# Kernel optimization log

Hardware: AMD Instinct MI355X
Metric: run time of the kernel (lower is better)

Reference implementation:

```python
import jax, jax.numpy as jnp
import numpy as np

N, C, B = 32, 1024, 1024
EPS = 1e-12


def setup_inputs() -> dict:
    key = jax.random.key(0)
    k1, k2, k3 = jax.random.split(key, 3)
    X = jax.random.normal(k1, (N, C, B), dtype=jnp.float32)
    # xavier_uniform for square [C, C]: bound = sqrt(6/(C+C))
    bound = float(np.sqrt(6.0 / (C + C)))
    Wk = jax.random.uniform(k2, (C, C), minval=-bound, maxval=bound, dtype=jnp.float32)
    Wq = jax.random.uniform(k3, (C, C), minval=-bound, maxval=bound, dtype=jnp.float32)
    Wk0 = jnp.zeros((C, 1), dtype=jnp.float32)
    Wq0 = jnp.zeros((C, 1), dtype=jnp.float32)
    return {"X": X, "Wk": Wk, "Wq": Wq, "Wk0": Wk0, "Wq0": Wq0}


def reference(X, Wk, Wq, Wk0, Wq0):
    # X: [N, C, B]; Wk/Wq: [C, C]; Wk0/Wq0: [C, 1]
    K = jnp.einsum('cd,ndb->ncb', Wk, X) + Wk0  # [N, C, B]
    Q = jnp.einsum('cd,ndb->ncb', Wq, X) + Wq0  # [N, C, B]
    DK2 = jnp.sum(K * K, axis=1)                # [N, B]
    DQ2 = jnp.sum(Q * Q, axis=1)                # [N, B]
    DQK = jnp.sqrt(jnp.maximum(DQ2[:, :, None] * DK2[:, None, :], EPS))  # [N, B, B]
    Y = jnp.einsum('ncq,nck->nqk', Q, K) / DQK  # [N, B, B]
    SM = jax.nn.softmax(Y, axis=1)              # column-wise softmax (dim=1)
    Z = jnp.einsum('ncb,nbq->ncq', X, SM)       # [N, C, B]
    return Z
```

## Files before the change

kernel.cpp:

```cpp
#include <hip/hip_runtime.h>


typedef __bf16 bf16x8 __attribute__((ext_vector_type(8)));
typedef float  f32x4  __attribute__((ext_vector_type(4)));

#define LOAD16_LDS(g, l)                                                       \
  __builtin_amdgcn_global_load_lds(                                            \
      (const __attribute__((address_space(1))) void*)(g),                      \
      (__attribute__((address_space(3))) void*)(l), 16, 0, 0)

#define FENCE() asm volatile("" ::: "memory")
#define SBAR()                                                                 \
  do { FENCE(); __builtin_amdgcn_s_barrier(); FENCE(); } while (0)
#define LGKM0()                                                                \
  do { asm volatile("s_waitcnt lgkmcnt(0)" ::: "memory");                      \
       __builtin_amdgcn_sched_barrier(0); } while (0)
#define VMW(n)                                                                 \
  do { asm volatile("s_waitcnt vmcnt(" #n ")" ::: "memory");                   \
       __builtin_amdgcn_sched_barrier(0); } while (0)
#define MFMA16(a, b, c) __builtin_amdgcn_mfma_f32_16x16x32_bf16((a), (b), (c), 0, 0, 0)

__global__ __launch_bounds__(256) void convert_w(
    const float* __restrict__ Wk, const float* __restrict__ Wq,
    const float* __restrict__ Wk0, const float* __restrict__ Wq0,
    __bf16* __restrict__ Wb, float* __restrict__ bias2) {
  int i = blockIdx.x * 256 + threadIdx.x;
  if (i < 1048576) Wb[i] = (__bf16)Wk[i];
  else             Wb[i] = (__bf16)Wq[i - 1048576];
  if (i < 1024) bias2[i] = Wk0[i];
  if (i >= 1048576 && i < 1048576 + 1024) bias2[1024 + (i - 1048576)] = Wq0[i - 1048576];
}

__global__ __launch_bounds__(256) void convert_x(
    const float* __restrict__ X, __bf16* __restrict__ Xb, __bf16* __restrict__ Xtb) {
  const int n = blockIdx.z;
  const int c0 = blockIdx.y * 32, b0 = blockIdx.x * 32;
  __shared__ float t[32][33];
  const int tx = threadIdx.x, ty = threadIdx.y;
  const float* Xn = X + (size_t)n * 1024 * 1024;
  __bf16* Xbn = Xb + (size_t)n * 1024 * 1024;
  __bf16* Xtn = Xtb + (size_t)n * 1024 * 1024;
#pragma unroll
  for (int i = 0; i < 4; ++i) {
    int c = c0 + ty + i * 8;
    float v = Xn[(size_t)c * 1024 + b0 + tx];
    Xbn[(size_t)c * 1024 + b0 + tx] = (__bf16)v;
    t[ty + i * 8][tx] = v;
  }
  __syncthreads();
#pragma unroll
  for (int i = 0; i < 4; ++i) {
    int b = b0 + ty + i * 8;
    Xtn[(size_t)b * 1024 + c0 + tx] = (__bf16)t[tx][ty + i * 8];
  }
}

template <int EPI>
__global__ __launch_bounds__(512) void gemm256(
    const __bf16* __restrict__ A, const __bf16* __restrict__ Bm,
    void* __restrict__ Out, int lda, int ldb, int ldo, int K,
    long long sA, long long sB, long long sO,
    const float* __restrict__ rowS, const float* __restrict__ colS,
    const float* __restrict__ bias,
    float* __restrict__ sq0, float* __restrict__ sq1) {
  extern __shared__ char smem[];
  const int n = blockIdx.z;
  A += (size_t)n * sA;
  Bm += (size_t)n * sB;
  const int tileM = blockIdx.y * 256, tileN = blockIdx.x * 256;

  const int tid = threadIdx.x;
  const int w = tid >> 6, lane = tid & 63;
  const int wm = w >> 2, wn = w & 3;
  const int r16 = lane & 15, q16 = lane >> 4;
  const int wb = w * 1024;

  const int srow = tid >> 3;
  const int scol8 = ((tid & 7) ^ (srow & 7)) * 8;
  const __bf16* gA[4];
  const __bf16* gB[4];
#pragma unroll
  for (int c = 0; c < 4; ++c) {
    gA[c] = A + (size_t)(tileM + c * 64 + srow) * lda + scol8;
    gB[c] = Bm + (size_t)(tileN + c * 64 + srow) * ldb + scol8;
  }

  const int sw = (r16 & 7) << 4;
  const int cc0 = (q16 * 16) ^ sw;
  const int cc1 = cc0 ^ 64;
  const int aRow = (wm * 128 + r16) * 128;
  const int bRow = (wn * 64 + r16) * 128;

  f32x4 acc[8][4];
#pragma unroll
  for (int i = 0; i < 8; ++i)
#pragma unroll
    for (int j = 0; j < 4; ++j) acc[i][j] = (f32x4){0.f, 0.f, 0.f, 0.f};

  const int NT = K >> 6;

  {
    char* A0 = smem;
    char* B0 = smem + 32768;
    char* A1 = smem + 65536;
    char* B1 = smem + 65536 + 32768;
    LOAD16_LDS(gB[0], B0 + 0 * 8192 + wb);
    LOAD16_LDS(gB[1], B0 + 1 * 8192 + wb);
    FENCE();
    LOAD16_LDS(gB[2], B0 + 2 * 8192 + wb);
    LOAD16_LDS(gB[3], B0 + 3 * 8192 + wb);
    FENCE();
    LOAD16_LDS(gA[0], A0 + 0 * 8192 + wb);
    LOAD16_LDS(gA[2], A0 + 2 * 8192 + wb);
    FENCE();
    LOAD16_LDS(gA[1], A0 + 1 * 8192 + wb);
    LOAD16_LDS(gA[3], A0 + 3 * 8192 + wb);
    FENCE();
    LOAD16_LDS(gB[0] + 64, B1 + 0 * 8192 + wb);
    LOAD16_LDS(gB[1] + 64, B1 + 1 * 8192 + wb);
    FENCE();
    LOAD16_LDS(gB[2] + 64, B1 + 2 * 8192 + wb);
    LOAD16_LDS(gB[3] + 64, B1 + 3 * 8192 + wb);
    FENCE();
    LOAD16_LDS(gA[0] + 64, A1 + 0 * 8192 + wb);
    LOAD16_LDS(gA[2] + 64, A1 + 2 * 8192 + wb);
    VMW(6);
    SBAR();
  }

  int kU3 = 64, kU0 = 128, kU1 = 128, kU2 = 128;

  for (int t = 0; t < NT; ++t) {
    char* Ab = smem + (size_t)((t & 1) * 65536);
    char* Bb = Ab + 32768;
    char* An = smem + (size_t)(((t & 1) ^ 1) * 65536);

    bf16x8 bfr[4][2];
#pragma unroll
    for (int ni = 0; ni < 4; ++ni) {
      bfr[ni][0] = *(const bf16x8*)(Bb + bRow + ni * 2048 + cc0);
      bfr[ni][1] = *(const bf16x8*)(Bb + bRow + ni * 2048 + cc1);
    }

#pragma unroll
    for (int p = 0; p < 4; ++p) {
      bf16x8 af[2][2];
#pragma unroll
      for (int j = 0; j < 2; ++j) {
        af[j][0] = *(const bf16x8*)(Ab + aRow + (2 * p + j) * 2048 + cc0);
        af[j][1] = *(const bf16x8*)(Ab + aRow + (2 * p + j) * 2048 + cc1);
      }
      if (p == 0) {
        if (kU3 < K) {
          LOAD16_LDS(gA[1] + kU3, An + 1 * 8192 + wb);
          LOAD16_LDS(gA[3] + kU3, An + 3 * 8192 + wb);
          kU3 += 64;
        }
      } else if (p == 1) {
        if (kU0 < K) {
          LOAD16_LDS(gB[0] + kU0, Bb + 0 * 8192 + wb);
          LOAD16_LDS(gB[1] + kU0, Bb + 1 * 8192 + wb);
          kU0 += 64;
        }
      } else if (p == 2) {
        if (kU1 < K) {
          LOAD16_LDS(gB[2] + kU1, Bb + 2 * 8192 + wb);
          LOAD16_LDS(gB[3] + kU1, Bb + 3 * 8192 + wb);
          kU1 += 64;
        }
      } else {
        if (kU2 < K) {
          LOAD16_LDS(gA[0] + kU2, Ab + 0 * 8192 + wb);
          LOAD16_LDS(gA[2] + kU2, Ab + 2 * 8192 + wb);
          kU2 += 64;
        }
        if (t < NT - 2) { VMW(6); } else { VMW(0); }
      }
      SBAR();
      LGKM0();
      __builtin_amdgcn_s_setprio(1);
#pragma unroll
      for (int ni = 0; ni < 4; ++ni) {
#pragma unroll
        for (int j = 0; j < 2; ++j) {
          acc[2 * p + j][ni] = MFMA16(af[j][0], bfr[ni][0], acc[2 * p + j][ni]);
          acc[2 * p + j][ni] = MFMA16(af[j][1], bfr[ni][1], acc[2 * p + j][ni]);
        }
      }
      __builtin_amdgcn_s_setprio(0);
      SBAR();
    }
  }

  const int rowBase = tileM + wm * 128;
  const int colBase = tileN + wn * 64;
  if (EPI == 0) {
    float* sqp = (tileN < 1024) ? sq0 : sq1;
    float bs[4];
#pragma unroll
    for (int ni = 0; ni < 4; ++ni) bs[ni] = bias[colBase + ni * 16 + r16];
#pragma unroll
    for (int mi = 0; mi < 8; ++mi) {
#pragma unroll
      for (int t_ = 0; t_ < 4; ++t_) {
        const int grow = rowBase + mi * 16 + q16 * 4 + t_;
        float ss = 0.f;
#pragma unroll
        for (int ni = 0; ni < 4; ++ni) {
          const int gcol = colBase + ni * 16 + r16;
          const __bf16 bv = (__bf16)(acc[mi][ni][t_] + bs[ni]);
          ((__bf16*)Out)[(size_t)n * sO + (size_t)grow * ldo + gcol] = bv;
          const float f = (float)bv;
          ss += f * f;
        }
        ss += __shfl_xor(ss, 1);
        ss += __shfl_xor(ss, 2);
        ss += __shfl_xor(ss, 4);
        ss += __shfl_xor(ss, 8);
        if (r16 == 0) atomicAdd(&sqp[n * 1024 + grow], ss);
      }
    }
  } else if (EPI == 1) {
    float cs[4];
#pragma unroll
    for (int ni = 0; ni < 4; ++ni)
      cs[ni] = colS[n * 1024 + colBase + ni * 16 + r16];
#pragma unroll
    for (int mi = 0; mi < 8; ++mi) {
#pragma unroll
      for (int t_ = 0; t_ < 4; ++t_) {
        const int grow = rowBase + mi * 16 + q16 * 4 + t_;
        const float rs = rowS[n * 1024 + grow];
        float ss = 0.f;
#pragma unroll
        for (int ni = 0; ni < 4; ++ni) {
          const int gcol = colBase + ni * 16 + r16;
          const float y = acc[mi][ni][t_] * rsqrtf(fmaxf(rs * cs[ni], 1e-12f));
          const __bf16 e = (__bf16)__expf(y - 1.0f);
          ((__bf16*)Out)[(size_t)n * sO + (size_t)grow * ldo + gcol] = e;
          ss += (float)e;
        }
        ss += __shfl_xor(ss, 1);
        ss += __shfl_xor(ss, 2);
        ss += __shfl_xor(ss, 4);
        ss += __shfl_xor(ss, 8);
        if (r16 == 0) atomicAdd(&sq0[n * 1024 + grow], ss);
      }
    }
  } else {
    float inv[4];
#pragma unroll
    for (int ni = 0; ni < 4; ++ni)
      inv[ni] = 1.0f / colS[n * 1024 + colBase + ni * 16 + r16];
#pragma unroll
    for (int mi = 0; mi < 8; ++mi)
#pragma unroll
      for (int ni = 0; ni < 4; ++ni)
#pragma unroll
        for (int t_ = 0; t_ < 4; ++t_) {
          const int grow = rowBase + mi * 16 + q16 * 4 + t_;
          const int gcol = colBase + ni * 16 + r16;
          ((float*)Out)[(size_t)n * sO + (size_t)grow * ldo + gcol] =
              acc[mi][ni][t_] * inv[ni];
        }
  }
}

extern "C" void kernel_launch(void* const* d_in, const int* in_sizes, int n_in,
                              void* d_out, int out_size, void* d_ws, size_t ws_size,
                              hipStream_t stream) {
  const float* X   = (const float*)d_in[0];
  const float* Wk  = (const float*)d_in[1];
  const float* Wq  = (const float*)d_in[2];
  const float* Wk0 = (const float*)d_in[3];
  const float* Wq0 = (const float*)d_in[4];

  char* ws = (char*)d_ws;
  const size_t MB = 1ull << 20;
  __bf16* Xb   = (__bf16*)(ws);
  __bf16* Xtb  = (__bf16*)(ws + 64 * MB);
  __bf16* ET   = (__bf16*)(ws + 64 * MB);
  __bf16* Wb   = (__bf16*)(ws + 128 * MB);
  __bf16* KQT  = (__bf16*)(ws + 132 * MB);
  float*  DK2  = (float*)(ws + 260 * MB);
  float*  DQ2  = (float*)(ws + 260 * MB + 128 * 1024);
  float*  S    = (float*)(ws + 260 * MB + 256 * 1024);
  float*  bias2= (float*)(ws + 260 * MB + 384 * 1024);

  const long long M1 = 1024LL * 1024LL;

  hipFuncSetAttribute(reinterpret_cast<const void*>(&gemm256<0>),
                      hipFuncAttributeMaxDynamicSharedMemorySize, 131072);
  hipFuncSetAttribute(reinterpret_cast<const void*>(&gemm256<1>),
                      hipFuncAttributeMaxDynamicSharedMemorySize, 131072);
  hipFuncSetAttribute(reinterpret_cast<const void*>(&gemm256<2>),
                      hipFuncAttributeMaxDynamicSharedMemorySize, 131072);

  hipMemsetAsync(DK2, 0, 3 * 128 * 1024, stream);

  convert_w<<<8192, 256, 0, stream>>>(Wk, Wq, Wk0, Wq0, Wb, bias2);
  convert_x<<<dim3(32, 32, 32), dim3(32, 8), 0, stream>>>(X, Xb, Xtb);

  gemm256<0><<<dim3(8, 4, 32), 512, 131072, stream>>>(
      Xtb, Wb, KQT, 1024, 1024, 2048, 1024, M1, 0LL, 2 * M1,
      nullptr, nullptr, bias2, DK2, DQ2);

  gemm256<1><<<dim3(4, 4, 32), 512, 131072, stream>>>(
      KQT, KQT + 1024, ET, 2048, 2048, 1024, 1024, 2 * M1, 2 * M1, M1,
      DK2, DQ2, nullptr, S, nullptr);

  gemm256<2><<<dim3(4, 4, 32), 512, 131072, stream>>>(
      Xb, ET, (float*)d_out, 1024, 1024, 1024, 1024, M1, M1, M1,
      nullptr, S, nullptr, nullptr, nullptr);
}
```

Baseline: 580.9 us.

## Make GEMM blocks persistent over several N-tiles with cross-tile prefetch

Each GEMM block now processes IPB consecutive output tiles along N, launched as a flat grid of 256 blocks (one per CU). During the last K iteration of one tile, it prefetches the first K-slices of the next tile's B and A operands into the free LDS buffer, so the next tile's pipeline starts warm and the epilogue overlaps with loading. This cuts the number of waves and the pipeline ramp-up per tile, and keeps the A row tile resident across iterations. The trade-off is a serial chain of tiles per block, with a full vmcnt wait after each epilogue and more fragile waitcnt accounting.

```diff
diff --git a/kernel.cpp b/kernel.cpp
--- a/kernel.cpp
+++ b/kernel.cpp
@@ -55,7 +55,7 @@
   }
 }
 
-template <int EPI>
+template <int EPI, int IPB, int GXS>
 __global__ __launch_bounds__(512) void gemm256(
     const __bf16* __restrict__ A, const __bf16* __restrict__ Bm,
     void* __restrict__ Out, int lda, int ldb, int ldo, int K,
@@ -64,10 +64,14 @@
     const float* __restrict__ bias,
     float* __restrict__ sq0, float* __restrict__ sq1) {
   extern __shared__ char smem[];
-  const int n = blockIdx.z;
+
+  const int baseid = blockIdx.x * IPB;
+  const int tN0   = (baseid & ((1 << GXS) - 1)) * 256;
+  const int tileM = ((baseid >> GXS) & 3) * 256;
+  const int n     = baseid >> (GXS + 2);
+
   A += (size_t)n * sA;
   Bm += (size_t)n * sB;
-  const int tileM = blockIdx.y * 256, tileN = blockIdx.x * 256;
 
   const int tid = threadIdx.x;
   const int w = tid >> 6, lane = tid & 63;
@@ -82,8 +86,9 @@
 #pragma unroll
   for (int c = 0; c < 4; ++c) {
     gA[c] = A + (size_t)(tileM + c * 64 + srow) * lda + scol8;
-    gB[c] = Bm + (size_t)(tileN + c * 64 + srow) * ldb + scol8;
+    gB[c] = Bm + (size_t)(tN0 + c * 64 + srow) * ldb + scol8;
   }
+  const long long bStep = 256LL * ldb;
 
   const int sw = (r16 & 7) << 4;
   const int cc0 = (q16 * 16) ^ sw;
@@ -91,178 +96,215 @@
   const int aRow = (wm * 128 + r16) * 128;
   const int bRow = (wn * 64 + r16) * 128;
 
-  f32x4 acc[8][4];
-#pragma unroll
-  for (int i = 0; i < 8; ++i)
-#pragma unroll
-    for (int j = 0; j < 4; ++j) acc[i][j] = (f32x4){0.f, 0.f, 0.f, 0.f};
-
   const int NT = K >> 6;
 
-  {
+#pragma unroll 1
+  for (int it = 0; it < IPB; ++it) {
+    const int tileN = tN0 + it * 256;
+    const bool pre = (it + 1 < IPB);
+
+    f32x4 acc[8][4];
+#pragma unroll
+    for (int i = 0; i < 8; ++i)
+#pragma unroll
+      for (int j = 0; j < 4; ++j) acc[i][j] = (f32x4){0.f, 0.f, 0.f, 0.f};
+
     char* A0 = smem;
     char* B0 = smem + 32768;
     char* A1 = smem + 65536;
     char* B1 = smem + 65536 + 32768;
-    LOAD16_LDS(gB[0], B0 + 0 * 8192 + wb);
-    LOAD16_LDS(gB[1], B0 + 1 * 8192 + wb);
-    FENCE();
-    LOAD16_LDS(gB[2], B0 + 2 * 8192 + wb);
-    LOAD16_LDS(gB[3], B0 + 3 * 8192 + wb);
-    FENCE();
-    LOAD16_LDS(gA[0], A0 + 0 * 8192 + wb);
-    LOAD16_LDS(gA[2], A0 + 2 * 8192 + wb);
-    FENCE();
-    LOAD16_LDS(gA[1], A0 + 1 * 8192 + wb);
-    LOAD16_LDS(gA[3], A0 + 3 * 8192 + wb);
-    FENCE();
-    LOAD16_LDS(gB[0] + 64, B1 + 0 * 8192 + wb);
-    LOAD16_LDS(gB[1] + 64, B1 + 1 * 8192 + wb);
-    FENCE();
-    LOAD16_LDS(gB[2] + 64, B1 + 2 * 8192 + wb);
-    LOAD16_LDS(gB[3] + 64, B1 + 3 * 8192 + wb);
-    FENCE();
-    LOAD16_LDS(gA[0] + 64, A1 + 0 * 8192 + wb);
-    LOAD16_LDS(gA[2] + 64, A1 + 2 * 8192 + wb);
-    VMW(6);
-    SBAR();
-  }
-
-  int kU3 = 64, kU0 = 128, kU1 = 128, kU2 = 128;
-
-  for (int t = 0; t < NT; ++t) {
-    char* Ab = smem + (size_t)((t & 1) * 65536);
-    char* Bb = Ab + 32768;
-    char* An = smem + (size_t)(((t & 1) ^ 1) * 65536);
-
-    bf16x8 bfr[4][2];
-#pragma unroll
-    for (int ni = 0; ni < 4; ++ni) {
-      bfr[ni][0] = *(const bf16x8*)(Bb + bRow + ni * 2048 + cc0);
-      bfr[ni][1] = *(const bf16x8*)(Bb + bRow + ni * 2048 + cc1);
-    }
-
-#pragma unroll
-    for (int p = 0; p < 4; ++p) {
-      bf16x8 af[2][2];
-#pragma unroll
-      for (int j = 0; j < 2; ++j) {
-        af[j][0] = *(const bf16x8*)(Ab + aRow + (2 * p + j) * 2048 + cc0);
-        af[j][1] = *(const bf16x8*)(Ab + aRow + (2 * p + j) * 2048 + cc1);
-      }
-      if (p == 0) {
-        if (kU3 < K) {
-          LOAD16_LDS(gA[1] + kU3, An + 1 * 8192 + wb);
-          LOAD16_LDS(gA[3] + kU3, An + 3 * 8192 + wb);
-          kU3 += 64;
-        }
-      } else if (p == 1) {
-        if (kU0 < K) {
-          LOAD16_LDS(gB[0] + kU0, Bb + 0 * 8192 + wb);
-          LOAD16_LDS(gB[1] + kU0, Bb + 1 * 8192 + wb);
-          kU0 += 64;
-        }
-      } else if (p == 2) {
-        if (kU1 < K) {
-          LOAD16_LDS(gB[2] + kU1, Bb + 2 * 8192 + wb);
-          LOAD16_LDS(gB[3] + kU1, Bb + 3 * 8192 + wb);
-          kU1 += 64;
-        }
-      } else {
-        if (kU2 < K) {
-          LOAD16_LDS(gA[0] + kU2, Ab + 0 * 8192 + wb);
-          LOAD16_LDS(gA[2] + kU2, Ab + 2 * 8192 + wb);
-          kU2 += 64;
-        }
-        if (t < NT - 2) { VMW(6); } else { VMW(0); }
-      }
+
+    if (it == 0) {
+      LOAD16_LDS(gB[0], B0 + 0 * 8192 + wb);
+      LOAD16_LDS(gB[1], B0 + 1 * 8192 + wb);
+      FENCE();
+      LOAD16_LDS(gB[2], B0 + 2 * 8192 + wb);
+      LOAD16_LDS(gB[3], B0 + 3 * 8192 + wb);
+      FENCE();
+      LOAD16_LDS(gA[0], A0 + 0 * 8192 + wb);
+      LOAD16_LDS(gA[2], A0 + 2 * 8192 + wb);
+      FENCE();
+      LOAD16_LDS(gA[1], A0 + 1 * 8192 + wb);
+      LOAD16_LDS(gA[3], A0 + 3 * 8192 + wb);
+      FENCE();
+      LOAD16_LDS(gB[0] + 64, B1 + 0 * 8192 + wb);
+      LOAD16_LDS(gB[1] + 64, B1 + 1 * 8192 + wb);
+      FENCE();
+      LOAD16_LDS(gB[2] + 64, B1 + 2 * 8192 + wb);
+      LOAD16_LDS(gB[3] + 64, B1 + 3 * 8192 + wb);
+      FENCE();
+      LOAD16_LDS(gA[0] + 64, A1 + 0 * 8192 + wb);
+      LOAD16_LDS(gA[2] + 64, A1 + 2 * 8192 + wb);
+      VMW(6);
       SBAR();
-      LGKM0();
-      __builtin_amdgcn_s_setprio(1);
-#pragma unroll
-      for (int ni = 0; ni < 4; ++ni) {
-#pragma unroll
-        for (int j = 0; j < 2; ++j) {
-          acc[2 * p + j][ni] = MFMA16(af[j][0], bfr[ni][0], acc[2 * p + j][ni]);
-          acc[2 * p + j][ni] = MFMA16(af[j][1], bfr[ni][1], acc[2 * p + j][ni]);
-        }
-      }
-      __builtin_amdgcn_s_setprio(0);
+    } else {
+      LOAD16_LDS(gB[0] + 64, B1 + 0 * 8192 + wb);
+      LOAD16_LDS(gB[1] + 64, B1 + 1 * 8192 + wb);
+      FENCE();
+      LOAD16_LDS(gB[2] + 64, B1 + 2 * 8192 + wb);
+      LOAD16_LDS(gB[3] + 64, B1 + 3 * 8192 + wb);
+      FENCE();
+      LOAD16_LDS(gA[0] + 64, A1 + 0 * 8192 + wb);
+      LOAD16_LDS(gA[2] + 64, A1 + 2 * 8192 + wb);
       SBAR();
     }
-  }
-
-  const int rowBase = tileM + wm * 128;
-  const int colBase = tileN + wn * 64;
-  if (EPI == 0) {
-    float* sqp = (tileN < 1024) ? sq0 : sq1;
-    float bs[4];
-#pragma unroll
-    for (int ni = 0; ni < 4; ++ni) bs[ni] = bias[colBase + ni * 16 + r16];
-#pragma unroll
-    for (int mi = 0; mi < 8; ++mi) {
-#pragma unroll
-      for (int t_ = 0; t_ < 4; ++t_) {
-        const int grow = rowBase + mi * 16 + q16 * 4 + t_;
-        float ss = 0.f;
+
+    int kU3 = 64, kU0 = 128, kU1 = 128, kU2 = 128;
+
+    for (int t = 0; t < NT; ++t) {
+      char* Ab = smem + (size_t)((t & 1) * 65536);
+      char* Bb = Ab + 32768;
+      char* An = smem + (size_t)(((t & 1) ^ 1) * 65536);
+      char* Bn = An + 32768;
+
+      bf16x8 bfr[4][2];
+#pragma unroll
+      for (int ni = 0; ni < 4; ++ni) {
+        bfr[ni][0] = *(const bf16x8*)(Bb + bRow + ni * 2048 + cc0);
+        bfr[ni][1] = *(const bf16x8*)(Bb + bRow + ni * 2048 + cc1);
+      }
+
+#pragma unroll
+      for (int p = 0; p < 4; ++p) {
+        bf16x8 af[2][2];
+#pragma unroll
+        for (int j = 0; j < 2; ++j) {
+          af[j][0] = *(const bf16x8*)(Ab + aRow + (2 * p + j) * 2048 + cc0);
+          af[j][1] = *(const bf16x8*)(Ab + aRow + (2 * p + j) * 2048 + cc1);
+        }
+        if (p == 0) {
+          if (kU3 < K) {
+            LOAD16_LDS(gA[1] + kU3, An + 1 * 8192 + wb);
+            LOAD16_LDS(gA[3] + kU3, An + 3 * 8192 + wb);
+            kU3 += 64;
+          } else if (pre && t == NT - 1) {
+            LOAD16_LDS(gB[0] + bStep, Bn + 0 * 8192 + wb);
+            LOAD16_LDS(gB[1] + bStep, Bn + 1 * 8192 + wb);
+          }
+        } else if (p == 1) {
+          if (kU0 < K) {
+            LOAD16_LDS(gB[0] + kU0, Bb + 0 * 8192 + wb);
+            LOAD16_LDS(gB[1] + kU0, Bb + 1 * 8192 + wb);
+            kU0 += 64;
+          } else if (pre && t == NT - 1) {
+            LOAD16_LDS(gB[2] + bStep, Bn + 2 * 8192 + wb);
+            LOAD16_LDS(gB[3] + bStep, Bn + 3 * 8192 + wb);
+          }
+        } else if (p == 2) {
+          if (kU1 < K) {
+            LOAD16_LDS(gB[2] + kU1, Bb + 2 * 8192 + wb);
+            LOAD16_LDS(gB[3] + kU1, Bb + 3 * 8192 + wb);
+            kU1 += 64;
+          } else if (pre && t == NT - 1) {
+            LOAD16_LDS(gA[0], An + 0 * 8192 + wb);
+            LOAD16_LDS(gA[2], An + 2 * 8192 + wb);
+          }
+        } else {
+          if (kU2 < K) {
+            LOAD16_LDS(gA[0] + kU2, Ab + 0 * 8192 + wb);
+            LOAD16_LDS(gA[2] + kU2, Ab + 2 * 8192 + wb);
+            kU2 += 64;
+          } else if (pre && t == NT - 1) {
+            LOAD16_LDS(gA[1], An + 1 * 8192 + wb);
+            LOAD16_LDS(gA[3], An + 3 * 8192 + wb);
+          }
+          if (t <= NT - 3)      { VMW(6); }
+          else if (t == NT - 2) { VMW(0); }
+        }
+        SBAR();
+        LGKM0();
+        __builtin_amdgcn_s_setprio(1);
 #pragma unroll
         for (int ni = 0; ni < 4; ++ni) {
-          const int gcol = colBase + ni * 16 + r16;
-          const __bf16 bv = (__bf16)(acc[mi][ni][t_] + bs[ni]);
-          ((__bf16*)Out)[(size_t)n * sO + (size_t)grow * ldo + gcol] = bv;
-          const float f = (float)bv;
-          ss += f * f;
-        }
-        ss += __shfl_xor(ss, 1);
-        ss += __shfl_xor(ss, 2);
-        ss += __shfl_xor(ss, 4);
-        ss += __shfl_xor(ss, 8);
-        if (r16 == 0) atomicAdd(&sqp[n * 1024 + grow], ss);
+#pragma unroll
+          for (int j = 0; j < 2; ++j) {
+            acc[2 * p + j][ni] = MFMA16(af[j][0], bfr[ni][0], acc[2 * p + j][ni]);
+            acc[2 * p + j][ni] = MFMA16(af[j][1], bfr[ni][1], acc[2 * p + j][ni]);
+          }
+        }
+        __builtin_amdgcn_s_setprio(0);
+        SBAR();
       }
     }
-  } else if (EPI == 1) {
-    float cs[4];
-#pragma unroll
-    for (int ni = 0; ni < 4; ++ni)
-      cs[ni] = colS[n * 1024 + colBase + ni * 16 + r16];
-#pragma unroll
-    for (int mi = 0; mi < 8; ++mi) {
-#pragma unroll
-      for (int t_ = 0; t_ < 4; ++t_) {
-        const int grow = rowBase + mi * 16 + q16 * 4 + t_;
-        const float rs = rowS[n * 1024 + grow];
-        float ss = 0.f;
-#pragma unroll
-        for (int ni = 0; ni < 4; ++ni) {
-          const int gcol = colBase + ni * 16 + r16;
-          const float y = acc[mi][ni][t_] * rsqrtf(fmaxf(rs * cs[ni], 1e-12f));
-          const __bf16 e = (__bf16)__expf(y - 1.0f);
-          ((__bf16*)Out)[(size_t)n * sO + (size_t)grow * ldo + gcol] = e;
-          ss += (float)e;
-        }
-        ss += __shfl_xor(ss, 1);
-        ss += __shfl_xor(ss, 2);
-        ss += __shfl_xor(ss, 4);
-        ss += __shfl_xor(ss, 8);
-        if (r16 == 0) atomicAdd(&sq0[n * 1024 + grow], ss);
-      }
-    }
-  } else {
-    float inv[4];
-#pragma unroll
-    for (int ni = 0; ni < 4; ++ni)
-      inv[ni] = 1.0f / colS[n * 1024 + colBase + ni * 16 + r16];
-#pragma unroll
-    for (int mi = 0; mi < 8; ++mi)
-#pragma unroll
-      for (int ni = 0; ni < 4; ++ni)
+
+    const int rowBase = tileM + wm * 128;
+    const int colBase = tileN + wn * 64;
+    if (EPI == 0) {
+      float* sqp = (tileN < 1024) ? sq0 : sq1;
+      float bs[4];
+#pragma unroll
+      for (int ni = 0; ni < 4; ++ni) bs[ni] = bias[colBase + ni * 16 + r16];
+#pragma unroll
+      for (int mi = 0; mi < 8; ++mi) {
 #pragma unroll
         for (int t_ = 0; t_ < 4; ++t_) {
           const int grow = rowBase + mi * 16 + q16 * 4 + t_;
-          const int gcol = colBase + ni * 16 + r16;
-          ((float*)Out)[(size_t)n * sO + (size_t)grow * ldo + gcol] =
-              acc[mi][ni][t_] * inv[ni];
-        }
+          float ss = 0.f;
+#pragma unroll
+          for (int ni = 0; ni < 4; ++ni) {
+            const int gcol = colBase + ni * 16 + r16;
+            const __bf16 bv = (__bf16)(acc[mi][ni][t_] + bs[ni]);
+            ((__bf16*)Out)[(size_t)n * sO + (size_t)grow * ldo + gcol] = bv;
+            const float f = (float)bv;
+            ss += f * f;
+          }
+          ss += __shfl_xor(ss, 1);
+          ss += __shfl_xor(ss, 2);
+          ss += __shfl_xor(ss, 4);
+          ss += __shfl_xor(ss, 8);
+          if (r16 == 0) atomicAdd(&sqp[n * 1024 + grow], ss);
+        }
+      }
+    } else if (EPI == 1) {
+      float cs[4];
+#pragma unroll
+      for (int ni = 0; ni < 4; ++ni)
+        cs[ni] = colS[n * 1024 + colBase + ni * 16 + r16];
+#pragma unroll
+      for (int mi = 0; mi < 8; ++mi) {
+#pragma unroll
+        for (int t_ = 0; t_ < 4; ++t_) {
+          const int grow = rowBase + mi * 16 + q16 * 4 + t_;
+          const float rs = rowS[n * 1024 + grow];
+          float ss = 0.f;
+#pragma unroll
+          for (int ni = 0; ni < 4; ++ni) {
+            const int gcol = colBase + ni * 16 + r16;
+            const float y = acc[mi][ni][t_] * rsqrtf(fmaxf(rs * cs[ni], 1e-12f));
+            const __bf16 e = (__bf16)__expf(y - 1.0f);
+            ((__bf16*)Out)[(size_t)n * sO + (size_t)grow * ldo + gcol] = e;
+            ss += (float)e;
+          }
+          ss += __shfl_xor(ss, 1);
+          ss += __shfl_xor(ss, 2);
+          ss += __shfl_xor(ss, 4);
+          ss += __shfl_xor(ss, 8);
+          if (r16 == 0) atomicAdd(&sq0[n * 1024 + grow], ss);
+        }
+      }
+    } else {
+      float inv[4];
+#pragma unroll
+      for (int ni = 0; ni < 4; ++ni)
+        inv[ni] = 1.0f / colS[n * 1024 + colBase + ni * 16 + r16];
+#pragma unroll
+      for (int mi = 0; mi < 8; ++mi)
+#pragma unroll
+        for (int ni = 0; ni < 4; ++ni)
+#pragma unroll
+          for (int t_ = 0; t_ < 4; ++t_) {
+            const int grow = rowBase + mi * 16 + q16 * 4 + t_;
+            const int gcol = colBase + ni * 16 + r16;
+            ((float*)Out)[(size_t)n * sO + (size_t)grow * ldo + gcol] =
+                acc[mi][ni][t_] * inv[ni];
+          }
+    }
+
+    if (pre) {
+      VMW(0);
+#pragma unroll
+      for (int c = 0; c < 4; ++c) gB[c] += bStep;
+    }
   }
 }
 
@@ -289,11 +331,11 @@
 
   const long long M1 = 1024LL * 1024LL;
 
-  hipFuncSetAttribute(reinterpret_cast<const void*>(&gemm256<0>),
+  hipFuncSetAttribute(reinterpret_cast<const void*>(&gemm256<0, 4, 3>),
                       hipFuncAttributeMaxDynamicSharedMemorySize, 131072);
-  hipFuncSetAttribute(reinterpret_cast<const void*>(&gemm256<1>),
+  hipFuncSetAttribute(reinterpret_cast<const void*>(&gemm256<1, 2, 2>),
                       hipFuncAttributeMaxDynamicSharedMemorySize, 131072);
-  hipFuncSetAttribute(reinterpret_cast<const void*>(&gemm256<2>),
+  hipFuncSetAttribute(reinterpret_cast<const void*>(&gemm256<2, 2, 2>),
                       hipFuncAttributeMaxDynamicSharedMemorySize, 131072);
 
   hipMemsetAsync(DK2, 0, 3 * 128 * 1024, stream);
@@ -301,15 +343,15 @@
   convert_w<<<8192, 256, 0, stream>>>(Wk, Wq, Wk0, Wq0, Wb, bias2);
   convert_x<<<dim3(32, 32, 32), dim3(32, 8), 0, stream>>>(X, Xb, Xtb);
 
-  gemm256<0><<<dim3(8, 4, 32), 512, 131072, stream>>>(
+  gemm256<0, 4, 3><<<dim3(256), 512, 131072, stream>>>(
       Xtb, Wb, KQT, 1024, 1024, 2048, 1024, M1, 0LL, 2 * M1,
       nullptr, nullptr, bias2, DK2, DQ2);
 
-  gemm256<1><<<dim3(4, 4, 32), 512, 131072, stream>>>(
+  gemm256<1, 2, 2><<<dim3(256), 512, 131072, stream>>>(
       KQT, KQT + 1024, ET, 2048, 2048, 1024, 1024, 2 * M1, 2 * M1, M1,
       DK2, DQ2, nullptr, S, nullptr);
 
-  gemm256<2><<<dim3(4, 4, 32), 512, 131072, stream>>>(
+  gemm256<2, 2, 2><<<dim3(256), 512, 131072, stream>>>(
       Xb, ET, (float*)d_out, 1024, 1024, 1024, 1024, M1, M1, M1,
       nullptr, S, nullptr, nullptr, nullptr);
 }
```

After: 659.0 us. +13.4%, slower.

## Pad bf16 workspace row strides and defer X conversion to reuse KQT buffer

Applied to the files above, without the earlier changes.

Row strides of the bf16 intermediates change from 1024/2048 to 1032/2056 elements, likely to break power-of-two strides that cause cache-set or channel conflicts in the GEMM tile loads. The plain bf16 copy of X is split out of the transpose kernel into a separate vectorised kernel. That kernel runs after the second GEMM so its output can overwrite the now-dead KQT buffer and shrink the workspace. The cost is an extra launch and a second read of X.

```diff
diff --git a/kernel.cpp b/kernel.cpp
--- a/kernel.cpp
+++ b/kernel.cpp
@@ -20,6 +20,11 @@
        __builtin_amdgcn_sched_barrier(0); } while (0)
 #define MFMA16(a, b, c) __builtin_amdgcn_mfma_f32_16x16x32_bf16((a), (b), (c), 0, 0, 0)
 
+#define LDX 1032
+#define LDK 2056
+#define SX  (1024LL * LDX)
+#define SK  (1024LL * LDK)
+
 __global__ __launch_bounds__(256) void convert_w(
     const float* __restrict__ Wk, const float* __restrict__ Wq,
     const float* __restrict__ Wk0, const float* __restrict__ Wq0,
@@ -32,27 +37,34 @@
 }
 
 __global__ __launch_bounds__(256) void convert_x(
-    const float* __restrict__ X, __bf16* __restrict__ Xb, __bf16* __restrict__ Xtb) {
+    const float* __restrict__ X, __bf16* __restrict__ Xtb) {
   const int n = blockIdx.z;
   const int c0 = blockIdx.y * 32, b0 = blockIdx.x * 32;
   __shared__ float t[32][33];
   const int tx = threadIdx.x, ty = threadIdx.y;
   const float* Xn = X + (size_t)n * 1024 * 1024;
-  __bf16* Xbn = Xb + (size_t)n * 1024 * 1024;
-  __bf16* Xtn = Xtb + (size_t)n * 1024 * 1024;
+  __bf16* Xtn = Xtb + (size_t)n * SX;
 #pragma unroll
   for (int i = 0; i < 4; ++i) {
     int c = c0 + ty + i * 8;
-    float v = Xn[(size_t)c * 1024 + b0 + tx];
-    Xbn[(size_t)c * 1024 + b0 + tx] = (__bf16)v;
-    t[ty + i * 8][tx] = v;
+    t[ty + i * 8][tx] = Xn[(size_t)c * 1024 + b0 + tx];
   }
   __syncthreads();
 #pragma unroll
   for (int i = 0; i < 4; ++i) {
     int b = b0 + ty + i * 8;
-    Xtn[(size_t)b * 1024 + c0 + tx] = (__bf16)t[tx][ty + i * 8];
-  }
+    Xtn[(size_t)b * LDX + c0 + tx] = (__bf16)t[tx][ty + i * 8];
+  }
+}
+
+__global__ __launch_bounds__(256) void convert_xb(
+    const float* __restrict__ X, __bf16* __restrict__ Xb) {
+  const int c = blockIdx.x, n = blockIdx.y;
+  const float* src = X + ((size_t)n * 1024 + c) * 1024 + threadIdx.x * 4;
+  __bf16* dst = Xb + (size_t)n * SX + (size_t)c * LDX + threadIdx.x * 4;
+  float4 v = *(const float4*)src;
+  __bf16 o[4] = {(__bf16)v.x, (__bf16)v.y, (__bf16)v.z, (__bf16)v.w};
+  *(ushort4*)dst = *(const ushort4*)o;
 }
 
 template <int EPI>
@@ -276,18 +288,15 @@
   const float* Wq0 = (const float*)d_in[4];
 
   char* ws = (char*)d_ws;
-  const size_t MB = 1ull << 20;
-  __bf16* Xb   = (__bf16*)(ws);
-  __bf16* Xtb  = (__bf16*)(ws + 64 * MB);
-  __bf16* ET   = (__bf16*)(ws + 64 * MB);
-  __bf16* Wb   = (__bf16*)(ws + 128 * MB);
-  __bf16* KQT  = (__bf16*)(ws + 132 * MB);
-  float*  DK2  = (float*)(ws + 260 * MB);
-  float*  DQ2  = (float*)(ws + 260 * MB + 128 * 1024);
-  float*  S    = (float*)(ws + 260 * MB + 256 * 1024);
-  float*  bias2= (float*)(ws + 260 * MB + 384 * 1024);
-
-  const long long M1 = 1024LL * 1024LL;
+  float*  DK2  = (float*)(ws);
+  float*  DQ2  = (float*)(ws + 131072);
+  float*  S    = (float*)(ws + 262144);
+  float*  bias2= (float*)(ws + 393216);
+  __bf16* Xtb  = (__bf16*)(ws + 524288);
+  __bf16* ET   = (__bf16*)(ws + 524288);
+  __bf16* Wb   = (__bf16*)(ws + 68157440ull);
+  __bf16* KQT  = (__bf16*)(ws + 72351744ull);
+  __bf16* Xb   = (__bf16*)(ws + 72351744ull);
 
   hipFuncSetAttribute(reinterpret_cast<const void*>(&gemm256<0>),
                       hipFuncAttributeMaxDynamicSharedMemorySize, 131072);
@@ -296,20 +305,22 @@
   hipFuncSetAttribute(reinterpret_cast<const void*>(&gemm256<2>),
                       hipFuncAttributeMaxDynamicSharedMemorySize, 131072);
 
-  hipMemsetAsync(DK2, 0, 3 * 128 * 1024, stream);
+  hipMemsetAsync(DK2, 0, 3 * 131072, stream);
 
   convert_w<<<8192, 256, 0, stream>>>(Wk, Wq, Wk0, Wq0, Wb, bias2);
-  convert_x<<<dim3(32, 32, 32), dim3(32, 8), 0, stream>>>(X, Xb, Xtb);
+  convert_x<<<dim3(32, 32, 32), dim3(32, 8), 0, stream>>>(X, Xtb);
 
   gemm256<0><<<dim3(8, 4, 32), 512, 131072, stream>>>(
-      Xtb, Wb, KQT, 1024, 1024, 2048, 1024, M1, 0LL, 2 * M1,
+      Xtb, Wb, KQT, LDX, 1024, LDK, 1024, SX, 0LL, SK,
       nullptr, nullptr, bias2, DK2, DQ2);
 
   gemm256<1><<<dim3(4, 4, 32), 512, 131072, stream>>>(
-      KQT, KQT + 1024, ET, 2048, 2048, 1024, 1024, 2 * M1, 2 * M1, M1,
+      KQT, KQT + 1024, ET, LDK, LDK, LDX, 1024, SK, SK, SX,
       DK2, DQ2, nullptr, S, nullptr);
 
+  convert_xb<<<dim3(1024, 32), 256, 0, stream>>>(X, Xb);
+
   gemm256<2><<<dim3(4, 4, 32), 512, 131072, stream>>>(
-      Xb, ET, (float*)d_out, 1024, 1024, 1024, 1024, M1, M1, M1,
+      Xb, ET, (float*)d_out, LDX, LDX, 1024, 1024, SX, SX, 1024LL * 1024LL,
       nullptr, S, nullptr, nullptr, nullptr);
 }
```

After: 643.9 us. 1.11x slower.

## Run the K/Q projection and QK^T GEMMs in FP8 instead of BF16

Applied to the files above, without the earlier changes.

Converts W and transposed X to FP8 e4m3 and adds a new FP8 MFMA GEMM kernel, with a 64-byte K tile and a different LDS swizzle, for the projection and score GEMMs. The K/Q intermediate is also stored in FP8. The final X·softmax GEMM stays BF16. This halves the operand bytes and uses the higher-throughput FP8 MFMA, at the cost of much lower precision in the normalized dot products, which feed an exp and may hurt accuracy.

```diff
diff --git a/kernel.cpp b/kernel.cpp
--- a/kernel.cpp
+++ b/kernel.cpp
@@ -19,27 +19,32 @@
   do { asm volatile("s_waitcnt vmcnt(" #n ")" ::: "memory");                   \
        __builtin_amdgcn_sched_barrier(0); } while (0)
 #define MFMA16(a, b, c) __builtin_amdgcn_mfma_f32_16x16x32_bf16((a), (b), (c), 0, 0, 0)
+#define MFMA8(a, b, c)  __builtin_amdgcn_mfma_f32_16x16x32_fp8_fp8((a), (b), (c), 0, 0, 0)
+
+#define F32_TO_FP8PK(a, b) __builtin_amdgcn_cvt_pk_fp8_f32((a), (b), 0, false)
+#define FP8_TO_F32(p, s)   __builtin_amdgcn_cvt_f32_fp8((p), (s))
 
 __global__ __launch_bounds__(256) void convert_w(
     const float* __restrict__ Wk, const float* __restrict__ Wq,
     const float* __restrict__ Wk0, const float* __restrict__ Wq0,
-    __bf16* __restrict__ Wb, float* __restrict__ bias2) {
+    unsigned char* __restrict__ W8, float* __restrict__ bias2) {
   int i = blockIdx.x * 256 + threadIdx.x;
-  if (i < 1048576) Wb[i] = (__bf16)Wk[i];
-  else             Wb[i] = (__bf16)Wq[i - 1048576];
+  float v = (i < 1048576) ? Wk[i] : Wq[i - 1048576];
+  W8[i] = (unsigned char)(F32_TO_FP8PK(v, v) & 0xff);
   if (i < 1024) bias2[i] = Wk0[i];
   if (i >= 1048576 && i < 1048576 + 1024) bias2[1024 + (i - 1048576)] = Wq0[i - 1048576];
 }
 
 __global__ __launch_bounds__(256) void convert_x(
-    const float* __restrict__ X, __bf16* __restrict__ Xb, __bf16* __restrict__ Xtb) {
+    const float* __restrict__ X, __bf16* __restrict__ Xb,
+    unsigned char* __restrict__ Xt8) {
   const int n = blockIdx.z;
   const int c0 = blockIdx.y * 32, b0 = blockIdx.x * 32;
   __shared__ float t[32][33];
   const int tx = threadIdx.x, ty = threadIdx.y;
   const float* Xn = X + (size_t)n * 1024 * 1024;
   __bf16* Xbn = Xb + (size_t)n * 1024 * 1024;
-  __bf16* Xtn = Xtb + (size_t)n * 1024 * 1024;
+  unsigned char* Xtn = Xt8 + (size_t)n * 1024 * 1024;
 #pragma unroll
   for (int i = 0; i < 4; ++i) {
     int c = c0 + ty + i * 8;
@@ -51,13 +56,14 @@
 #pragma unroll
   for (int i = 0; i < 4; ++i) {
     int b = b0 + ty + i * 8;
-    Xtn[(size_t)b * 1024 + c0 + tx] = (__bf16)t[tx][ty + i * 8];
+    float v = t[tx][ty + i * 8];
+    Xtn[(size_t)b * 1024 + c0 + tx] = (unsigned char)(F32_TO_FP8PK(v, v) & 0xff);
   }
 }
 
 template <int EPI>
-__global__ __launch_bounds__(512) void gemm256(
-    const __bf16* __restrict__ A, const __bf16* __restrict__ Bm,
+__global__ __launch_bounds__(512) void gemm_fp8(
+    const unsigned char* __restrict__ A, const unsigned char* __restrict__ Bm,
     void* __restrict__ Out, int lda, int ldb, int ldo, int K,
     long long sA, long long sB, long long sO,
     const float* __restrict__ rowS, const float* __restrict__ colS,
@@ -69,8 +75,171 @@
   Bm += (size_t)n * sB;
   const int tileM = blockIdx.y * 256, tileN = blockIdx.x * 256;
 
-  const int tid = threadIdx.x;
-  const int w = tid >> 6, lane = tid & 63;
+  const int tid = threadIdx.x, w = tid >> 6, lane = tid & 63;
+  const int wm = w >> 2, wn = w & 3;
+  const int r16 = lane & 15, q16 = lane >> 4;
+
+  const int hf = w >> 2, wq = w & 3;
+  const int srow = wq * 16 + (lane >> 2);
+  const int scol = (((lane & 3) ^ ((lane >> 2) & 3) ^ ((lane >> 4) & 3)) << 4);
+  const unsigned char* gA2 = A + (size_t)(tileM + hf * 128 + srow) * lda + scol;
+  const unsigned char* gA3 = A + (size_t)(tileM + 64 + hf * 128 + srow) * lda + scol;
+  const unsigned char* gB0 = Bm + (size_t)(tileN + hf * 64 + srow) * ldb + scol;
+  const unsigned char* gB1 = Bm + (size_t)(tileN + 128 + hf * 64 + srow) * ldb + scol;
+  const int dA2 = hf * 8192 + wq * 1024;
+  const int dA3 = dA2 + 4096;
+  const int dB0 = hf * 4096 + wq * 1024;
+  const int dB1 = dB0 + 8192;
+
+  const int s16 = (r16 & 3) ^ ((r16 >> 2) & 3);
+  const int cc0 = (((q16 >> 1) ^ s16) << 4) + ((q16 & 1) << 3);
+  const int cc1 = cc0 ^ 32;
+  const int aRow = (wm * 128 + r16) * 64;
+  const int bRow = (wn * 64 + r16) * 64;
+
+  f32x4 acc[8][4];
+#pragma unroll
+  for (int i = 0; i < 8; ++i)
+#pragma unroll
+    for (int j = 0; j < 4; ++j) acc[i][j] = (f32x4){0.f, 0.f, 0.f, 0.f};
+
+  const int NT = K >> 6;
+
+  {
+    char* A0 = smem;
+    char* B0 = smem + 16384;
+    char* A1 = smem + 32768;
+    char* B1 = A1 + 16384;
+    LOAD16_LDS(gB0, B0 + dB0); FENCE();
+    LOAD16_LDS(gB1, B0 + dB1); FENCE();
+    LOAD16_LDS(gA2, A0 + dA2); FENCE();
+    LOAD16_LDS(gA3, A0 + dA3); FENCE();
+    LOAD16_LDS(gB0 + 64, B1 + dB0); FENCE();
+    LOAD16_LDS(gB1 + 64, B1 + dB1); FENCE();
+    LOAD16_LDS(gA2 + 64, A1 + dA2);
+    VMW(3);
+    SBAR();
+  }
+
+  int kU3 = 64, kU0 = 128, kU1 = 128, kU2 = 128;
+
+  for (int t = 0; t < NT; ++t) {
+    char* Ab = smem + (size_t)((t & 1) * 32768);
+    char* Bb = Ab + 16384;
+    char* An = smem + (size_t)(((t & 1) ^ 1) * 32768);
+
+    long bfr[4][2];
+#pragma unroll
+    for (int ni = 0; ni < 4; ++ni) {
+      bfr[ni][0] = *(const long*)(Bb + bRow + ni * 1024 + cc0);
+      bfr[ni][1] = *(const long*)(Bb + bRow + ni * 1024 + cc1);
+    }
+
+#pragma unroll
+    for (int p = 0; p < 4; ++p) {
+      long af[2][2];
+#pragma unroll
+      for (int j = 0; j < 2; ++j) {
+        af[j][0] = *(const long*)(Ab + aRow + (2 * p + j) * 1024 + cc0);
+        af[j][1] = *(const long*)(Ab + aRow + (2 * p + j) * 1024 + cc1);
+      }
+      if (p == 0) {
+        if (kU3 < K) { LOAD16_LDS(gA3 + kU3, An + dA3); kU3 += 64; }
+      } else if (p == 1) {
+        if (kU0 < K) { LOAD16_LDS(gB0 + kU0, Bb + dB0); kU0 += 64; }
+      } else if (p == 2) {
+        if (kU1 < K) { LOAD16_LDS(gB1 + kU1, Bb + dB1); kU1 += 64; }
+      } else {
+        if (kU2 < K) { LOAD16_LDS(gA2 + kU2, Ab + dA2); kU2 += 64; }
+        if (t < NT - 2) { VMW(3); } else { VMW(0); }
+      }
+      SBAR();
+      LGKM0();
+      __builtin_amdgcn_s_setprio(1);
+#pragma unroll
+      for (int ni = 0; ni < 4; ++ni) {
+#pragma unroll
+        for (int j = 0; j < 2; ++j) {
+          acc[2 * p + j][ni] = MFMA8(af[j][0], bfr[ni][0], acc[2 * p + j][ni]);
+          acc[2 * p + j][ni] = MFMA8(af[j][1], bfr[ni][1], acc[2 * p + j][ni]);
+        }
+      }
+      __builtin_amdgcn_s_setprio(0);
+      SBAR();
+    }
+  }
+
+  const int rowBase = tileM + wm * 128;
+  const int colBase = tileN + wn * 64;
+  if (EPI == 0) {
+    float* sqp = (tileN < 1024) ? sq0 : sq1;
+    float bs[4];
+#pragma unroll
+    for (int ni = 0; ni < 4; ++ni) bs[ni] = bias[colBase + ni * 16 + r16];
+#pragma unroll
+    for (int mi = 0; mi < 8; ++mi) {
+#pragma unroll
+      for (int t_ = 0; t_ < 4; ++t_) {
+        const int grow = rowBase + mi * 16 + q16 * 4 + t_;
+        const int p01 = F32_TO_FP8PK(acc[mi][0][t_] + bs[0], acc[mi][1][t_] + bs[1]);
+        const int p23 = F32_TO_FP8PK(acc[mi][2][t_] + bs[2], acc[mi][3][t_] + bs[3]);
+        unsigned char* orow = (unsigned char*)Out + (size_t)n * sO + (size_t)grow * ldo;
+        orow[colBase + 0 * 16 + r16] = (unsigned char)(p01 & 0xff);
+        orow[colBase + 1 * 16 + r16] = (unsigned char)((p01 >> 8) & 0xff);
+        orow[colBase + 2 * 16 + r16] = (unsigned char)(p23 & 0xff);
+        orow[colBase + 3 * 16 + r16] = (unsigned char)((p23 >> 8) & 0xff);
+        const float f0 = FP8_TO_F32(p01, 0), f1 = FP8_TO_F32(p01, 1);
+        const float f2 = FP8_TO_F32(p23, 0), f3 = FP8_TO_F32(p23, 1);
+        float ss = f0 * f0 + f1 * f1 + f2 * f2 + f3 * f3;
+        ss += __shfl_xor(ss, 1);
+        ss += __shfl_xor(ss, 2);
+        ss += __shfl_xor(ss, 4);
+        ss += __shfl_xor(ss, 8);
+        if (r16 == 0) atomicAdd(&sqp[n * 1024 + grow], ss);
+      }
+    }
+  } else {
+    float cs[4];
+#pragma unroll
+    for (int ni = 0; ni < 4; ++ni)
+      cs[ni] = colS[n * 1024 + colBase + ni * 16 + r16];
+#pragma unroll
+    for (int mi = 0; mi < 8; ++mi) {
+#pragma unroll
+      for (int t_ = 0; t_ < 4; ++t_) {
+        const int grow = rowBase + mi * 16 + q16 * 4 + t_;
+        const float rs = rowS[n * 1024 + grow];
+        float ss = 0.f;
+#pragma unroll
+        for (int ni = 0; ni < 4; ++ni) {
+          const int gcol = colBase + ni * 16 + r16;
+          const float y = acc[mi][ni][t_] * rsqrtf(fmaxf(rs * cs[ni], 1e-12f));
+          const __bf16 e = (__bf16)__expf(y - 1.0f);
+          ((__bf16*)Out)[(size_t)n * sO + (size_t)grow * ldo + gcol] = e;
+          ss += (float)e;
+        }
+        ss += __shfl_xor(ss, 1);
+        ss += __shfl_xor(ss, 2);
+        ss += __shfl_xor(ss, 4);
+        ss += __shfl_xor(ss, 8);
+        if (r16 == 0) atomicAdd(&sq0[n * 1024 + grow], ss);
+      }
+    }
+  }
+}
+
+__global__ __launch_bounds__(512) void gemm256(
+    const __bf16* __restrict__ A, const __bf16* __restrict__ Bm,
+    float* __restrict__ Out, int lda, int ldb, int ldo, int K,
+    long long sA, long long sB, long long sO,
+    const float* __restrict__ colS) {
+  extern __shared__ char smem[];
+  const int n = blockIdx.z;
+  A += (size_t)n * sA;
+  Bm += (size_t)n * sB;
+  const int tileM = blockIdx.y * 256, tileN = blockIdx.x * 256;
+
+  const int tid = threadIdx.x, w = tid >> 6, lane = tid & 63;
   const int wm = w >> 2, wn = w & 3;
   const int r16 = lane & 15, q16 = lane >> 4;
   const int wb = w * 1024;
@@ -194,76 +363,20 @@
 
   const int rowBase = tileM + wm * 128;
   const int colBase = tileN + wn * 64;
-  if (EPI == 0) {
-    float* sqp = (tileN < 1024) ? sq0 : sq1;
-    float bs[4];
-#pragma unroll
-    for (int ni = 0; ni < 4; ++ni) bs[ni] = bias[colBase + ni * 16 + r16];
-#pragma unroll
-    for (int mi = 0; mi < 8; ++mi) {
+  float inv[4];
+#pragma unroll
+  for (int ni = 0; ni < 4; ++ni)
+    inv[ni] = 1.0f / colS[n * 1024 + colBase + ni * 16 + r16];
+#pragma unroll
+  for (int mi = 0; mi < 8; ++mi)
+#pragma unroll
+    for (int ni = 0; ni < 4; ++ni)
 #pragma unroll
       for (int t_ = 0; t_ < 4; ++t_) {
         const int grow = rowBase + mi * 16 + q16 * 4 + t_;
-        float ss = 0.f;
-#pragma unroll
-        for (int ni = 0; ni < 4; ++ni) {
-          const int gcol = colBase + ni * 16 + r16;
-          const __bf16 bv = (__bf16)(acc[mi][ni][t_] + bs[ni]);
-          ((__bf16*)Out)[(size_t)n * sO + (size_t)grow * ldo + gcol] = bv;
-          const float f = (float)bv;
-          ss += f * f;
-        }
-        ss += __shfl_xor(ss, 1);
-        ss += __shfl_xor(ss, 2);
-        ss += __shfl_xor(ss, 4);
-        ss += __shfl_xor(ss, 8);
-        if (r16 == 0) atomicAdd(&sqp[n * 1024 + grow], ss);
-      }
-    }
-  } else if (EPI == 1) {
-    float cs[4];
-#pragma unroll
-    for (int ni = 0; ni < 4; ++ni)
-      cs[ni] = colS[n * 1024 + colBase + ni * 16 + r16];
-#pragma unroll
-    for (int mi = 0; mi < 8; ++mi) {
-#pragma unroll
-      for (int t_ = 0; t_ < 4; ++t_) {
-        const int grow = rowBase + mi * 16 + q16 * 4 + t_;
-        const float rs = rowS[n * 1024 + grow];
-        float ss = 0.f;
-#pragma unroll
-        for (int ni = 0; ni < 4; ++ni) {
-          const int gcol = colBase + ni * 16 + r16;
-          const float y = acc[mi][ni][t_] * rsqrtf(fmaxf(rs * cs[ni], 1e-12f));
-          const __bf16 e = (__bf16)__expf(y - 1.0f);
-          ((__bf16*)Out)[(size_t)n * sO + (size_t)grow * ldo + gcol] = e;
-          ss += (float)e;
-        }
-        ss += __shfl_xor(ss, 1);
-        ss += __shfl_xor(ss, 2);
-        ss += __shfl_xor(ss, 4);
-        ss += __shfl_xor(ss, 8);
-        if (r16 == 0) atomicAdd(&sq0[n * 1024 + grow], ss);
-      }
-    }
-  } else {
-    float inv[4];
-#pragma unroll
-    for (int ni = 0; ni < 4; ++ni)
-      inv[ni] = 1.0f / colS[n * 1024 + colBase + ni * 16 + r16];
-#pragma unroll
-    for (int mi = 0; mi < 8; ++mi)
-#pragma unroll
-      for (int ni = 0; ni < 4; ++ni)
-#pragma unroll
-        for (int t_ = 0; t_ < 4; ++t_) {
-          const int grow = rowBase + mi * 16 + q16 * 4 + t_;
-          const int gcol = colBase + ni * 16 + r16;
-          ((float*)Out)[(size_t)n * sO + (size_t)grow * ldo + gcol] =
-              acc[mi][ni][t_] * inv[ni];
-        }
-  }
+        const int gcol = colBase + ni * 16 + r16;
+        Out[(size_t)n * sO + (size_t)grow * ldo + gcol] = acc[mi][ni][t_] * inv[ni];
+      }
 }
 
 extern "C" void kernel_launch(void* const* d_in, const int* in_sizes, int n_in,
@@ -277,39 +390,38 @@
 
   char* ws = (char*)d_ws;
   const size_t MB = 1ull << 20;
-  __bf16* Xb   = (__bf16*)(ws);
-  __bf16* Xtb  = (__bf16*)(ws + 64 * MB);
-  __bf16* ET   = (__bf16*)(ws + 64 * MB);
-  __bf16* Wb   = (__bf16*)(ws + 128 * MB);
-  __bf16* KQT  = (__bf16*)(ws + 132 * MB);
-  float*  DK2  = (float*)(ws + 260 * MB);
-  float*  DQ2  = (float*)(ws + 260 * MB + 128 * 1024);
-  float*  S    = (float*)(ws + 260 * MB + 256 * 1024);
-  float*  bias2= (float*)(ws + 260 * MB + 384 * 1024);
+  __bf16*        Xb   = (__bf16*)(ws);
+  unsigned char* Xt8  = (unsigned char*)(ws + 64 * MB);
+  __bf16*        ET   = (__bf16*)(ws + 96 * MB);
+  unsigned char* W8   = (unsigned char*)(ws + 160 * MB);
+  unsigned char* KQT8 = (unsigned char*)(ws + 162 * MB);
+  float*  DK2  = (float*)(ws + 226 * MB);
+  float*  DQ2  = (float*)(ws + 226 * MB + 128 * 1024);
+  float*  S    = (float*)(ws + 226 * MB + 256 * 1024);
+  float*  bias2= (float*)(ws + 226 * MB + 384 * 1024);
 
   const long long M1 = 1024LL * 1024LL;
 
-  hipFuncSetAttribute(reinterpret_cast<const void*>(&gemm256<0>),
+  hipFuncSetAttribute(reinterpret_cast<const void*>(&gemm_fp8<0>),
+                      hipFuncAttributeMaxDynamicSharedMemorySize, 65536);
+  hipFuncSetAttribute(reinterpret_cast<const void*>(&gemm_fp8<1>),
+                      hipFuncAttributeMaxDynamicSharedMemorySize, 65536);
+  hipFuncSetAttribute(reinterpret_cast<const void*>(&gemm256),
                       hipFuncAttributeMaxDynamicSharedMemorySize, 131072);
-  hipFuncSetAttribute(reinterpret_cast<const void*>(&gemm256<1>),
-                      hipFuncAttributeMaxDynamicSharedMemorySize, 131072);
-  hipFuncSetAttribute(reinterpret_cast<const void*>(&gemm256<2>),
-                      hipFuncAttributeMaxDynamicSharedMemorySize, 131072);
 
   hipMemsetAsync(DK2, 0, 3 * 128 * 1024, stream);
 
-  convert_w<<<8192, 256, 0, stream>>>(Wk, Wq, Wk0, Wq0, Wb, bias2);
-  convert_x<<<dim3(32, 32, 32), dim3(32, 8), 0, stream>>>(X, Xb, Xtb);
-
-  gemm256<0><<<dim3(8, 4, 32), 512, 131072, stream>>>(
-      Xtb, Wb, KQT, 1024, 1024, 2048, 1024, M1, 0LL, 2 * M1,
+  convert_w<<<8192, 256, 0, stream>>>(Wk, Wq, Wk0, Wq0, W8, bias2);
+  convert_x<<<dim3(32, 32, 32), dim3(32, 8), 0, stream>>>(X, Xb, Xt8);
+
+  gemm_fp8<0><<<dim3(8, 4, 32), 512, 65536, stream>>>(
+      Xt8, W8, KQT8, 1024, 1024, 2048, 1024, M1, 0LL, 2 * M1,
       nullptr, nullptr, bias2, DK2, DQ2);
 
-  gemm256<1><<<dim3(4, 4, 32), 512, 131072, stream>>>(
-      KQT, KQT + 1024, ET, 2048, 2048, 1024, 1024, 2 * M1, 2 * M1, M1,
+  gemm_fp8<1><<<dim3(4, 4, 32), 512, 65536, stream>>>(
+      KQT8, KQT8 + 1024, ET, 2048, 2048, 1024, 1024, 2 * M1, 2 * M1, M1,
       DK2, DQ2, nullptr, S, nullptr);
 
-  gemm256<2><<<dim3(4, 4, 32), 512, 131072, stream>>>(
-      Xb, ET, (float*)d_out, 1024, 1024, 1024, 1024, M1, M1, M1,
-      nullptr, S, nullptr, nullptr, nullptr);
+  gemm256<<<dim3(4, 4, 32), 512, 131072, stream>>>(
+      Xb, ET, (float*)d_out, 1024, 1024, 1024, 1024, M1, M1, M1, S);
 }
```

New measurement: 563.8 us. -2.9%, faster.
